# Kernel optimization log

Measured on AMD Instinct MI355X. Metric: run time of the kernel, lower is better.

The kernel has to match this reference:

```python
import jax, jax.numpy as jnp
import numpy as np

B, N, D, H, W, C = 2, 4, 48, 28, 60, 64
DOWNSAMPLE = 8
NX, NY, NZ = 192, 192, 1   # from size=(192,192), scale=0.25; zbound=[-10,10,20] -> nz=1
SCALE = 0.25
OFFSETX = 0
DMIN, DMAX, DSTEP = 2.0, 50.0, 1.0


def setup_inputs() -> dict:
    key = jax.random.key(0)
    x = jax.random.normal(key, (B, N, D, H, W, C), dtype=jnp.float32)
    ogfW, ogfH = W * DOWNSAMPLE, H * DOWNSAMPLE
    fx = fy = 250.0
    K = jnp.array([[fx, 0.0, ogfW / 2.0], [0.0, fy, ogfH / 2.0], [0.0, 0.0, 1.0]], jnp.float32)
    intrinsics = jnp.broadcast_to(K, (B, N, 3, 3))
    # camera->ego rotation: cam z (forward) -> ego x, cam x (right) -> ego -y, cam y (down) -> ego -z
    R = jnp.array([[0.0, 0.0, 1.0], [-1.0, 0.0, 0.0], [0.0, -1.0, 0.0]], jnp.float32)
    pose = jnp.zeros((B, N, 4, 4), jnp.float32)
    pose = pose.at[..., :3, :3].set(R)
    pose = pose.at[..., :3, 3].set(jnp.array([1.0, 0.0, 1.6], jnp.float32))
    pose = pose.at[..., 3, 3].set(1.0)
    return {"x": x, "intrinsics": intrinsics, "pose": pose}


def _frustum():
    # (D,H,W,3) frustum of (u*d, v*d, d) homogeneous pixel coords scaled by depth
    ds = jnp.arange(DMIN, DMAX, DSTEP, dtype=jnp.float32)          # (D,)
    xs = jnp.linspace(0.0, W * DOWNSAMPLE - 1, W, dtype=jnp.float32)
    ys = jnp.linspace(0.0, H * DOWNSAMPLE - 1, H, dtype=jnp.float32)
    d = jnp.broadcast_to(ds[:, None, None], (D, H, W))
    u = jnp.broadcast_to(xs[None, None, :], (D, H, W))
    v = jnp.broadcast_to(ys[None, :, None], (D, H, W))
    return jnp.stack([u * d, v * d, d], axis=-1)


def reference(x, intrinsics, pose):
    rots = pose[..., :3, :3]                 # (B,N,3,3)
    trans = pose[..., :3, 3]                 # (B,N,3)
    pts = _frustum()                         # (D,H,W,3)
    combine = rots @ jnp.linalg.inv(intrinsics)  # (B,N,3,3)
    # ego-frame point cloud: (B,N,D,H,W,3)
    geom = jnp.einsum('bnij,dhwj->bndhwi', combine, pts) + trans[:, :, None, None, None, :]
    # bev_intrinsics from bev_params_to_intrinsics(size, scale, offsetx)
    f_bev = 1.0 / SCALE
    cx_bev = NX / 2.0 + OFFSETX
    cy_bev = NY / 2.0
    # torch .long() truncates toward zero, same as astype(int32)
    gx = (geom[..., 0] * f_bev + cx_bev).astype(jnp.int32)
    gy = (geom[..., 1] * f_bev + cy_bev).astype(jnp.int32)
    gz = ((geom[..., 2] + 10.0) / 20.0).astype(jnp.int32)  # (z - bx2 + dx2/2)/dx2, bx2=0, dx2=20
    b = jnp.broadcast_to(jnp.arange(B, dtype=jnp.int32)[:, None, None, None, None], gx.shape)
    kept = (gx >= 0) & (gx < NX) & (gy >= 0) & (gy < NY) & (gz >= 0) & (gz < NZ)
    # segment scatter-add == sort + cumsum-diff + scatter-set (ranks unique after reduction)
    flat = ((b * NZ + gz) * NY + gy) * NX + gx
    flat = jnp.where(kept, flat, 0).reshape(-1)
    xf = jnp.where(kept[..., None], x, jnp.zeros((), x.dtype)).reshape(-1, C)
    out = jnp.zeros((B * NZ * NY * NX, C), x.dtype).at[flat].add(xf)
    out = out.reshape(B, NZ, NY, NX, C)
    # final[b, :, z, y, x] layout then cat(unbind(dim=2), dim=1) -> (B, NZ*C, NY, NX)
    return out.transpose(0, 1, 4, 2, 3).reshape(B, NZ * C, NY, NX)
```

## Files before the change

kernel.cpp:

```cpp
#include <hip/hip_runtime.h>

#define BB 2
#define NN 4
#define DD 48
#define HH 28
#define WW 60
#define CC 64
#define NXg 192
#define NYg 192
#define NZg 1
#define DOWNS 8

constexpr int PTS    = BB * NN * DD * HH * WW;
constexpr int NCELLS = BB * NZg * NYg * NXg;
constexpr int NYX    = NYg * NXg;

__global__ void __launch_bounds__(256)
scatter_kernel(const float* __restrict__ x,
               const float* __restrict__ intr,
               const float* __restrict__ pose,
               float* __restrict__ outT) {
    int tid  = threadIdx.x;
    int lane = tid & 63;
    int p    = blockIdx.x * 256 + tid;

    int w = p % WW;
    int t = p / WW;
    int h = t % HH; t /= HH;
    int d = t % DD; t /= DD;
    int n = t % NN;
    int b = t / NN;

    const float* K  = intr + (size_t)(b * NN + n) * 9;
    const float* Pm = pose + (size_t)(b * NN + n) * 16;

    double k00 = K[0], k01 = K[1], k02 = K[2];
    double k10 = K[3], k11 = K[4], k12 = K[5];
    double k20 = K[6], k21 = K[7], k22 = K[8];

    double det = k00 * (k11 * k22 - k12 * k21)
               - k01 * (k10 * k22 - k12 * k20)
               + k02 * (k10 * k21 - k11 * k20);
    double id = 1.0 / det;
    double i00 = (k11 * k22 - k12 * k21) * id;
    double i01 = (k02 * k21 - k01 * k22) * id;
    double i02 = (k01 * k12 - k02 * k11) * id;
    double i10 = (k12 * k20 - k10 * k22) * id;
    double i11 = (k00 * k22 - k02 * k20) * id;
    double i12 = (k02 * k10 - k00 * k12) * id;
    double i20 = (k10 * k21 - k11 * k20) * id;
    double i21 = (k01 * k20 - k00 * k21) * id;
    double i22 = (k00 * k11 - k01 * k10) * id;

    double r00 = Pm[0],  r01 = Pm[1],  r02 = Pm[2],  tx = Pm[3];
    double r10 = Pm[4],  r11 = Pm[5],  r12 = Pm[6],  ty = Pm[7];
    double r20 = Pm[8],  r21 = Pm[9],  r22 = Pm[10], tz = Pm[11];

    double c00 = r00 * i00 + r01 * i10 + r02 * i20;
    double c01 = r00 * i01 + r01 * i11 + r02 * i21;
    double c02 = r00 * i02 + r01 * i12 + r02 * i22;
    double c10 = r10 * i00 + r11 * i10 + r12 * i20;
    double c11 = r10 * i01 + r11 * i11 + r12 * i21;
    double c12 = r10 * i02 + r11 * i12 + r12 * i22;
    double c20 = r20 * i00 + r21 * i10 + r22 * i20;
    double c21 = r20 * i01 + r21 * i11 + r22 * i21;
    double c22 = r20 * i02 + r21 * i12 + r22 * i22;

    double u   = (double)w * ((double)(WW * DOWNS - 1) / (double)(WW - 1));
    double v   = (double)h * ((double)(HH * DOWNS - 1) / (double)(HH - 1));
    double dep = 2.0 + (double)d;
    double px = u * dep, py = v * dep, pz = dep;

    double gxf = (c00 * px + c01 * py + c02 * pz + tx) * 4.0 + 96.0;
    double gyf = (c10 * px + c11 * py + c12 * pz + ty) * 4.0 + 96.0;
    double gzf = ((c20 * px + c21 * py + c22 * pz + tz) + 10.0) / 20.0;

    int gx = (int)gxf;
    int gy = (int)gyf;
    int gz = (int)gzf;

    bool kept = (gx >= 0) & (gx < NXg) & (gy >= 0) & (gy < NYg) &
                (gz >= 0) & (gz < NZg);

    int cell = kept ? (((b * NZg + gz) * NYg + gy) * NXg + gx) : -1;

    unsigned long long mask = __ballot(cell >= 0);
    if (mask == 0ULL) return;

    int base = p - lane;
    float acc = 0.f;
    int   cur = -1;
    while (mask) {
        int ks = __ffsll((long long)mask) - 1;
        mask &= mask - 1ULL;
        int ck = __shfl(cell, ks);
        float xv = x[(size_t)(base + ks) * CC + lane];
        if (ck != cur) {
            if (cur >= 0) atomicAdd(&outT[(size_t)cur * CC + lane], acc);
            cur = ck;
            acc = 0.f;
        }
        acc += xv;
    }
    atomicAdd(&outT[(size_t)cur * CC + lane], acc);
}

__global__ void __launch_bounds__(256)
transpose_kernel(const float* __restrict__ outT,
                 float* __restrict__ out) {
    __shared__ float tile[64][65];
    int tid      = threadIdx.x;
    int cellbase = blockIdx.x * 64;

    const float* src = outT + (size_t)cellbase * CC;
    #pragma unroll
    for (int i = 0; i < 16; ++i) {
        int idx = i * 256 + tid;
        tile[idx >> 6][idx & 63] = src[idx];
    }
    __syncthreads();

    int bb     = cellbase / NYX;
    int yxbase = cellbase % NYX;
    float* dst = out + (size_t)bb * CC * NYX + yxbase;
    #pragma unroll
    for (int i = 0; i < 16; ++i) {
        int idx = i * 256 + tid;
        int ch  = idx >> 6;
        int cl  = idx & 63;
        dst[(size_t)ch * NYX + cl] = tile[cl][ch];
    }
}

extern "C" void kernel_launch(void* const* d_in, const int* in_sizes, int n_in,
                              void* d_out, int out_size, void* d_ws, size_t ws_size,
                              hipStream_t stream) {
    const float* x    = (const float*)d_in[0];
    const float* intr = (const float*)d_in[1];
    const float* pose = (const float*)d_in[2];
    float* out = (float*)d_out;

    float* outT = (float*)d_ws;

    hipMemsetAsync(outT, 0, (size_t)NCELLS * CC * sizeof(float), stream);
    scatter_kernel<<<PTS / 256, 256, 0, stream>>>(x, intr, pose, outT);
    transpose_kernel<<<NCELLS / 64, 256, 0, stream>>>(outT, out);
}
```

Before: 276.3 us.

## Precompute camera coefficients once and batch gathered loads eight at a time

Moves the per-point 3x3 inverse and rotation product into a tiny setup kernel that writes 12 doubles per camera, and the scatter kernel reads them. The per-wave gather loop now extracts eight kept lanes at once and issues their eight row loads before doing the run-length accumulation, so several memory requests are in flight instead of one at a time. The projection is also refactored into one FMA chain scaled by depth. The cost is an extra kernel launch and more registers, and the reordered double arithmetic could change truncation at cell boundaries.

```diff
diff --git a/kernel.cpp b/kernel.cpp
--- a/kernel.cpp
+++ b/kernel.cpp
@@ -15,24 +15,13 @@
 constexpr int NCELLS = BB * NZg * NYg * NXg;
 constexpr int NYX    = NYg * NXg;
 
-__global__ void __launch_bounds__(256)
-scatter_kernel(const float* __restrict__ x,
-               const float* __restrict__ intr,
-               const float* __restrict__ pose,
-               float* __restrict__ outT) {
-    int tid  = threadIdx.x;
-    int lane = tid & 63;
-    int p    = blockIdx.x * 256 + tid;
-
-    int w = p % WW;
-    int t = p / WW;
-    int h = t % HH; t /= HH;
-    int d = t % DD; t /= DD;
-    int n = t % NN;
-    int b = t / NN;
-
-    const float* K  = intr + (size_t)(b * NN + n) * 9;
-    const float* Pm = pose + (size_t)(b * NN + n) * 16;
+__global__ void setup_kernel(const float* __restrict__ intr,
+                             const float* __restrict__ pose,
+                             double* __restrict__ coef) {
+    int i = threadIdx.x;
+    if (i >= BB * NN) return;
+    const float* K  = intr + (size_t)i * 9;
+    const float* Pm = pose + (size_t)i * 16;
 
     double k00 = K[0], k01 = K[1], k02 = K[2];
     double k10 = K[3], k11 = K[4], k12 = K[5];
@@ -56,24 +45,49 @@
     double r10 = Pm[4],  r11 = Pm[5],  r12 = Pm[6],  ty = Pm[7];
     double r20 = Pm[8],  r21 = Pm[9],  r22 = Pm[10], tz = Pm[11];
 
-    double c00 = r00 * i00 + r01 * i10 + r02 * i20;
-    double c01 = r00 * i01 + r01 * i11 + r02 * i21;
-    double c02 = r00 * i02 + r01 * i12 + r02 * i22;
-    double c10 = r10 * i00 + r11 * i10 + r12 * i20;
-    double c11 = r10 * i01 + r11 * i11 + r12 * i21;
-    double c12 = r10 * i02 + r11 * i12 + r12 * i22;
-    double c20 = r20 * i00 + r21 * i10 + r22 * i20;
-    double c21 = r20 * i01 + r21 * i11 + r22 * i21;
-    double c22 = r20 * i02 + r21 * i12 + r22 * i22;
+    double* c = coef + (size_t)i * 12;
+    c[0] = r00 * i00 + r01 * i10 + r02 * i20;
+    c[1] = r00 * i01 + r01 * i11 + r02 * i21;
+    c[2] = r00 * i02 + r01 * i12 + r02 * i22;
+    c[3] = r10 * i00 + r11 * i10 + r12 * i20;
+    c[4] = r10 * i01 + r11 * i11 + r12 * i21;
+    c[5] = r10 * i02 + r11 * i12 + r12 * i22;
+    c[6] = r20 * i00 + r21 * i10 + r22 * i20;
+    c[7] = r20 * i01 + r21 * i11 + r22 * i21;
+    c[8] = r20 * i02 + r21 * i12 + r22 * i22;
+    c[9]  = tx;
+    c[10] = ty;
+    c[11] = tz;
+}
+
+__global__ void __launch_bounds__(256)
+scatter_kernel(const float* __restrict__ x,
+               const double* __restrict__ coef,
+               float* __restrict__ outT) {
+    int tid  = threadIdx.x;
+    int lane = tid & 63;
+    int p    = blockIdx.x * 256 + tid;
+
+    int w  = p % WW;
+    int t  = p / WW;
+    int h  = t % HH; t /= HH;
+    int d  = t % DD;
+    int bn = t / DD;
+    int b  = bn / NN;
+
+    const double* cf = coef + (size_t)bn * 12;
 
     double u   = (double)w * ((double)(WW * DOWNS - 1) / (double)(WW - 1));
     double v   = (double)h * ((double)(HH * DOWNS - 1) / (double)(HH - 1));
     double dep = 2.0 + (double)d;
-    double px = u * dep, py = v * dep, pz = dep;
 
-    double gxf = (c00 * px + c01 * py + c02 * pz + tx) * 4.0 + 96.0;
-    double gyf = (c10 * px + c11 * py + c12 * pz + ty) * 4.0 + 96.0;
-    double gzf = ((c20 * px + c21 * py + c22 * pz + tz) + 10.0) / 20.0;
+    double rx = cf[0] * u + cf[1] * v + cf[2];
+    double ry = cf[3] * u + cf[4] * v + cf[5];
+    double rz = cf[6] * u + cf[7] * v + cf[8];
+
+    double gxf = (rx * dep + cf[9])  * 4.0 + 96.0;
+    double gyf = (ry * dep + cf[10]) * 4.0 + 96.0;
+    double gzf = ((rz * dep + cf[11]) + 10.0) / 20.0;
 
     int gx = (int)gxf;
     int gy = (int)gyf;
@@ -90,19 +104,39 @@
     int base = p - lane;
     float acc = 0.f;
     int   cur = -1;
+
     while (mask) {
-        int ks = __ffsll((long long)mask) - 1;
-        mask &= mask - 1ULL;
-        int ck = __shfl(cell, ks);
-        float xv = x[(size_t)(base + ks) * CC + lane];
-        if (ck != cur) {
-            if (cur >= 0) atomicAdd(&outT[(size_t)cur * CC + lane], acc);
-            cur = ck;
-            acc = 0.f;
+        int k[8], c[8];
+        #pragma unroll
+        for (int j = 0; j < 8; ++j) {
+            k[j] = __ffsll((long long)mask) - 1;
+            mask &= mask - 1ULL;
         }
-        acc += xv;
+        #pragma unroll
+        for (int j = 0; j < 8; ++j) {
+            int kj = k[j] >= 0 ? k[j] : 0;
+            int cj = __shfl(cell, kj);
+            c[j] = k[j] >= 0 ? cj : -1;
+        }
+        float val[8];
+        #pragma unroll
+        for (int j = 0; j < 8; ++j) {
+            int kj = k[j] >= 0 ? k[j] : 0;
+            val[j] = x[(size_t)(base + kj) * CC + lane];
+        }
+        #pragma unroll
+        for (int j = 0; j < 8; ++j) {
+            if (c[j] < 0) continue;
+            if (c[j] == cur) {
+                acc += val[j];
+            } else {
+                if (cur >= 0) atomicAdd(&outT[(size_t)cur * CC + lane], acc);
+                cur = c[j];
+                acc = val[j];
+            }
+        }
     }
-    atomicAdd(&outT[(size_t)cur * CC + lane], acc);
+    if (cur >= 0) atomicAdd(&outT[(size_t)cur * CC + lane], acc);
 }
 
 __global__ void __launch_bounds__(256)
@@ -140,9 +174,11 @@
     const float* pose = (const float*)d_in[2];
     float* out = (float*)d_out;
 
-    float* outT = (float*)d_ws;
+    double* coef = (double*)d_ws;
+    float*  outT = (float*)d_ws + 256;
 
     hipMemsetAsync(outT, 0, (size_t)NCELLS * CC * sizeof(float), stream);
-    scatter_kernel<<<PTS / 256, 256, 0, stream>>>(x, intr, pose, outT);
+    setup_kernel<<<1, 64, 0, stream>>>(intr, pose, coef);
+    scatter_kernel<<<PTS / 256, 256, 0, stream>>>(x, coef, outT);
     transpose_kernel<<<NCELLS / 64, 256, 0, stream>>>(outT, out);
 }
```

Result: faster. 270.6 us (-2.1%).
